# Performance work log

Measured on AMD Instinct MI355X. Metric: run time of the kernel, lower is better.

## Reference

```python
import jax, jax.numpy as jnp
import numpy as np

N_NODES = 50000


def setup_inputs() -> dict:
    key = jax.random.key(0)
    ks = jax.random.split(key, 6)
    d_in, d_out = 256, 256
    n_edges = 1_600_000
    x = jax.random.normal(ks[0], (N_NODES, d_in), dtype=jnp.float32)
    edge_index = jax.random.randint(ks[1], (2, n_edges), 0, N_NODES, dtype=jnp.int64)
    edge_attr = jax.random.normal(ks[2], (n_edges, 16), dtype=jnp.float32)  # unused by forward
    W1 = jax.random.normal(ks[3], (d_in, d_out), dtype=jnp.float32) * (1.0 / np.sqrt(d_in))
    b1 = jnp.zeros((d_out,), dtype=jnp.float32)
    W2 = jax.random.normal(ks[4], (d_out, d_out), dtype=jnp.float32) * (1.0 / np.sqrt(d_out))
    b2 = jnp.zeros((d_out,), dtype=jnp.float32)
    eps = jnp.zeros((1,), dtype=jnp.float32)  # train_eps=True, init 0
    return {"x": x, "edge_index": edge_index, "edge_attr": edge_attr,
            "W1": W1, "b1": b1, "W2": W2, "b2": b2, "eps": eps}


def reference(x, edge_index, edge_attr, W1, b1, W2, b2, eps):
    src, dst = edge_index[0], edge_index[1]
    # sum aggregation: agg[i] = sum_{(j->i) in E} x[j]
    agg = jax.ops.segment_sum(x[src], dst, num_segments=N_NODES)  # [N, d_in]
    h = (1.0 + eps[0]) * x + agg
    # MLP: Linear -> ReLU -> (dropout=0) -> Linear
    h = jax.nn.relu(h @ W1 + b1)
    out = h @ W2 + b2
    return out
```

## Files before the change

kernel.cpp:

```cpp
#include <hip/hip_runtime.h>
#include <stdint.h>

#define NODES 50000
#define D 256
#define MP 50048
#define NBUCK 196
#define CAP 10240
#define EPB 4096
#define HS_LD 264
#define CAST_BLOCKS 12500

typedef short bf16x8 __attribute__((ext_vector_type(8)));
typedef float f32x4 __attribute__((ext_vector_type(4)));

__device__ inline unsigned short f2b(float f) {
    unsigned int u = __float_as_uint(f);
    unsigned int r = (u + 0x7fffu + ((u >> 16) & 1u)) >> 16;
    return (unsigned short)r;
}

__device__ inline bool ei_is64(const int* ei) {
    return (ei[1] | ei[3] | ei[5] | ei[7]) == 0;
}
__device__ inline int ei_get(const int* __restrict__ ei, long long pos, bool is64) {
    return is64 ? ei[2 * pos] : ei[(int)pos];
}

__global__ __launch_bounds__(256) void prep_kernel(const float* __restrict__ x,
                                                   unsigned short* __restrict__ xb,
                                                   int* __restrict__ bcnt,
                                                   const float* __restrict__ W1,
                                                   const float* __restrict__ W2,
                                                   unsigned short* __restrict__ P1,
                                                   unsigned short* __restrict__ P2) {
    int blk = blockIdx.x;
    if (blk < CAST_BLOCKS) {
        if (blk == 0 && threadIdx.x < NBUCK) bcnt[threadIdx.x] = 0;
        int t = blk * 256 + threadIdx.x;
        float4 v = ((const float4*)x)[t];
        unsigned int lo = (unsigned int)f2b(v.x) | ((unsigned int)f2b(v.y) << 16);
        unsigned int hi = (unsigned int)f2b(v.z) | ((unsigned int)f2b(v.w) << 16);
        ((uint2*)xb)[t] = make_uint2(lo, hi);
    } else {
        int t = (blk - CAST_BLOCKS) * 256 + threadIdx.x;
        const float* W = (t < 8192) ? W1 : W2;
        unsigned short* P = (t < 8192) ? P1 : P2;
        int u = t & 8191;
        int lane = u & 63, nt = (u >> 6) & 15, s = u >> 10;
        int q = lane >> 4, n = nt * 16 + (lane & 15);
        int kbase = s * 32 + q * 8;
#pragma unroll
        for (int j = 0; j < 8; j++) P[u * 8 + j] = f2b(W[(kbase + j) * D + n]);
    }
}

__global__ __launch_bounds__(256) void partA_kernel(const int* __restrict__ ei, int E,
                                                    int* __restrict__ bcnt,
                                                    unsigned int* __restrict__ ebufT) {
    __shared__ int cnt[256];
    __shared__ int gbase[256];
    __shared__ int lcur[256];
    bool is64 = ei_is64(ei);
    int tid = threadIdx.x;
    cnt[tid] = 0;
    lcur[tid] = 0;
    __syncthreads();
    long long pairBase = ((long long)blockIdx.x * EPB) >> 1;
    unsigned int w[16];
    int bk[16];
#pragma unroll
    for (int r = 0; r < 8; r++) {
        long long pp = pairBase + (long long)r * 256 + tid;
        long long e0 = pp * 2;
        int s0 = 0, s1 = 0, d0 = 0, d1 = 0;
        bool v1 = (e0 + 1 < E), v0 = (e0 < E);
        if (v1) {
            if (is64) {
                uint4 sv = *(const uint4*)(ei + 4 * pp);
                uint4 dv = *(const uint4*)(ei + (size_t)2 * E + 4 * pp);
                s0 = (int)sv.x; s1 = (int)sv.z; d0 = (int)dv.x; d1 = (int)dv.z;
            } else {
                uint2 sv = *(const uint2*)(ei + 2 * pp);
                uint2 dv = *(const uint2*)(ei + (size_t)E + 2 * pp);
                s0 = (int)sv.x; s1 = (int)sv.y; d0 = (int)dv.x; d1 = (int)dv.y;
            }
        } else if (v0) {
            s0 = ei_get(ei, e0, is64);
            d0 = ei_get(ei, (long long)E + e0, is64);
        }
        bk[2 * r] = v0 ? (d0 >> 8) : -1;
        bk[2 * r + 1] = v1 ? (d1 >> 8) : -1;
        w[2 * r] = ((unsigned int)(d0 & 255) << 16) | (unsigned int)s0;
        w[2 * r + 1] = ((unsigned int)(d1 & 255) << 16) | (unsigned int)s1;
        if (v0) atomicAdd(&cnt[bk[2 * r]], 1);
        if (v1) atomicAdd(&cnt[bk[2 * r + 1]], 1);
    }
    __syncthreads();
    if (tid < NBUCK && cnt[tid] > 0) gbase[tid] = atomicAdd(&bcnt[tid], cnt[tid]);
    __syncthreads();
#pragma unroll
    for (int r = 0; r < 16; r++) {
        if (bk[r] >= 0) {
            int p = atomicAdd(&lcur[bk[r]], 1);
            ebufT[(size_t)bk[r] * CAP + gbase[bk[r]] + p] = w[r];
        }
    }
}

__global__ __launch_bounds__(256) void bscan_kernel(const int* __restrict__ bcnt,
                                                    int* __restrict__ bstart,
                                                    int* __restrict__ offs, int E) {
    __shared__ int buf[256];
    int tid = threadIdx.x;
    int v = (tid < NBUCK) ? bcnt[tid] : 0;
    buf[tid] = v;
    __syncthreads();
    for (int off = 1; off < 256; off <<= 1) {
        int xv = (tid >= off) ? buf[tid - off] : 0;
        __syncthreads();
        buf[tid] += xv;
        __syncthreads();
    }
    if (tid < NBUCK) bstart[tid] = buf[tid] - v;
    if (tid == 0) offs[NODES] = E;
}

__global__ __launch_bounds__(1024) void partB_kernel(const int* __restrict__ bcnt,
                                                     const int* __restrict__ bstart,
                                                     const unsigned int* __restrict__ ebufT,
                                                     int* __restrict__ offs,
                                                     int* __restrict__ ebuf) {
    __shared__ int ncnt[256];
    __shared__ int ncur[256];
    int b = blockIdx.x, tid = threadIdx.x;
    int n = bcnt[b];
    int base = bstart[b];
    if (tid < 256) ncnt[tid] = 0;
    __syncthreads();
    const unsigned int* reg = ebufT + (size_t)b * CAP;
    for (int i = tid; i < n; i += 1024) atomicAdd(&ncnt[reg[i] >> 16], 1);
    __syncthreads();
    int v = 0;
    if (tid < 256) {
        v = ncnt[tid];
        ncur[tid] = v;
    }
    __syncthreads();
    for (int off = 1; off < 256; off <<= 1) {
        int xv = 0;
        if (tid < 256 && tid >= off) xv = ncur[tid - off];
        __syncthreads();
        if (tid < 256) ncur[tid] += xv;
        __syncthreads();
    }
    if (tid < 256) {
        int excl = ncur[tid] - v;
        int node = b * 256 + tid;
        if (node < NODES) offs[node] = base + excl;
        ncur[tid] = excl;
    }
    __syncthreads();
    for (int i = tid; i < n; i += 1024) {
        unsigned int w = reg[i];
        int p = atomicAdd(&ncur[w >> 16], 1);
        ebuf[base + p] = (int)(w & 0xffffu);
    }
}

__device__ inline void upk_add(uint4 w, float* a) {
    a[0] += __uint_as_float(w.x << 16);
    a[1] += __uint_as_float(w.x & 0xffff0000u);
    a[2] += __uint_as_float(w.y << 16);
    a[3] += __uint_as_float(w.y & 0xffff0000u);
    a[4] += __uint_as_float(w.z << 16);
    a[5] += __uint_as_float(w.z & 0xffff0000u);
    a[6] += __uint_as_float(w.w << 16);
    a[7] += __uint_as_float(w.w & 0xffff0000u);
}

__global__ __launch_bounds__(256) void agg_kernel(const unsigned short* __restrict__ xb,
                                                  const int* __restrict__ offs,
                                                  const int* __restrict__ ebuf,
                                                  const float* __restrict__ eps,
                                                  unsigned short* __restrict__ h0) {
    int wv = (blockIdx.x * 256 + threadIdx.x) >> 6;
    int lane = threadIdx.x & 63;
    if (wv >= NODES) return;
    int half = lane >> 5;
    int l32 = lane & 31;
    float aA[8] = {0, 0, 0, 0, 0, 0, 0, 0};
    float aB[8] = {0, 0, 0, 0, 0, 0, 0, 0};
    int beg = offs[wv], end = offs[wv + 1];
    int j = beg;
    for (; j + 8 <= end; j += 8) {
        int i0 = ebuf[j + half];
        int i1 = ebuf[j + 2 + half];
        int i2 = ebuf[j + 4 + half];
        int i3 = ebuf[j + 6 + half];
        uint4 w0 = *(const uint4*)(xb + (size_t)i0 * D + l32 * 8);
        uint4 w1 = *(const uint4*)(xb + (size_t)i1 * D + l32 * 8);
        uint4 w2 = *(const uint4*)(xb + (size_t)i2 * D + l32 * 8);
        uint4 w3 = *(const uint4*)(xb + (size_t)i3 * D + l32 * 8);
        upk_add(w0, aA);
        upk_add(w1, aB);
        upk_add(w2, aA);
        upk_add(w3, aB);
    }
    for (; j + 2 <= end; j += 2) {
        int i0 = ebuf[j + half];
        uint4 w0 = *(const uint4*)(xb + (size_t)i0 * D + l32 * 8);
        upk_add(w0, aA);
    }
    if (j < end && half == 0) {
        int i0 = ebuf[j];
        uint4 w0 = *(const uint4*)(xb + (size_t)i0 * D + l32 * 8);
        upk_add(w0, aA);
    }
    float a[8];
#pragma unroll
    for (int i = 0; i < 8; i++) {
        a[i] = aA[i] + aB[i];
        a[i] += __shfl_xor(a[i], 32);
    }
    if (half == 0) {
        float scale = 1.0f + eps[0];
        uint4 v = *(const uint4*)(xb + (size_t)wv * D + l32 * 8);
        a[0] += scale * __uint_as_float(v.x << 16);
        a[1] += scale * __uint_as_float(v.x & 0xffff0000u);
        a[2] += scale * __uint_as_float(v.y << 16);
        a[3] += scale * __uint_as_float(v.y & 0xffff0000u);
        a[4] += scale * __uint_as_float(v.z << 16);
        a[5] += scale * __uint_as_float(v.z & 0xffff0000u);
        a[6] += scale * __uint_as_float(v.w << 16);
        a[7] += scale * __uint_as_float(v.w & 0xffff0000u);
        uint4 o;
        o.x = (unsigned int)f2b(a[0]) | ((unsigned int)f2b(a[1]) << 16);
        o.y = (unsigned int)f2b(a[2]) | ((unsigned int)f2b(a[3]) << 16);
        o.z = (unsigned int)f2b(a[4]) | ((unsigned int)f2b(a[5]) << 16);
        o.w = (unsigned int)f2b(a[6]) | ((unsigned int)f2b(a[7]) << 16);
        ((uint4*)(h0 + (size_t)wv * D))[l32] = o;
    }
}

__global__ __launch_bounds__(256) void gemm_fused_kernel(const unsigned short* __restrict__ A,
                                                         const unsigned short* __restrict__ P1,
                                                         const float* __restrict__ b1,
                                                         const unsigned short* __restrict__ P2,
                                                         const float* __restrict__ b2,
                                                         float* __restrict__ out, int Mvalid) {
    __shared__ unsigned short hs[64 * HS_LD];
    int wv = threadIdx.x >> 6;
    int lane = threadIdx.x & 63;
    int quad = lane >> 4, l16 = lane & 15;
    int mBase = blockIdx.x * 64;
    const bf16x8* B1v = (const bf16x8*)P1;
    const bf16x8* B2v = (const bf16x8*)P2;

    {
        f32x4 acc[4][4] = {};
#pragma unroll
        for (int ks = 0; ks < 8; ks++) {
            bf16x8 af[4], bf[4];
#pragma unroll
            for (int mi = 0; mi < 4; mi++) {
                int row = mBase + mi * 16 + l16;
                af[mi] = *(const bf16x8*)(A + (size_t)row * D + ks * 32 + quad * 8);
            }
#pragma unroll
            for (int ni = 0; ni < 4; ni++) bf[ni] = B1v[(ks * 16 + wv * 4 + ni) * 64 + lane];
#pragma unroll
            for (int mi = 0; mi < 4; mi++)
#pragma unroll
                for (int ni = 0; ni < 4; ni++)
                    acc[mi][ni] = __builtin_amdgcn_mfma_f32_16x16x32_bf16(af[mi], bf[ni],
                                                                          acc[mi][ni], 0, 0, 0);
        }
#pragma unroll
        for (int mi = 0; mi < 4; mi++)
#pragma unroll
            for (int ni = 0; ni < 4; ni++) {
                int col = wv * 64 + ni * 16 + l16;
                float bs = b1[col];
#pragma unroll
                for (int r = 0; r < 4; r++) {
                    int rl = mi * 16 + quad * 4 + r;
                    hs[rl * HS_LD + col] = f2b(fmaxf(acc[mi][ni][r] + bs, 0.0f));
                }
            }
    }
    __syncthreads();

    f32x4 acc[4][4] = {};
#pragma unroll
    for (int ks = 0; ks < 8; ks++) {
        bf16x8 af[4], bf[4];
#pragma unroll
        for (int mi = 0; mi < 4; mi++)
            af[mi] = *(const bf16x8*)(hs + (mi * 16 + l16) * HS_LD + ks * 32 + quad * 8);
#pragma unroll
        for (int ni = 0; ni < 4; ni++) bf[ni] = B2v[(ks * 16 + wv * 4 + ni) * 64 + lane];
#pragma unroll
        for (int mi = 0; mi < 4; mi++)
#pragma unroll
            for (int ni = 0; ni < 4; ni++)
                acc[mi][ni] =
                    __builtin_amdgcn_mfma_f32_16x16x32_bf16(af[mi], bf[ni], acc[mi][ni], 0, 0, 0);
    }
#pragma unroll
    for (int mi = 0; mi < 4; mi++)
#pragma unroll
        for (int ni = 0; ni < 4; ni++) {
            int col = wv * 64 + ni * 16 + l16;
            float bs = b2[col];
#pragma unroll
            for (int r = 0; r < 4; r++) {
                int row = mBase + mi * 16 + quad * 4 + r;
                if (row < Mvalid) out[(size_t)row * D + col] = acc[mi][ni][r] + bs;
            }
        }
}

extern "C" void kernel_launch(void* const* d_in, const int* in_sizes, int n_in,
                              void* d_out, int out_size, void* d_ws, size_t ws_size,
                              hipStream_t stream) {
    const float* x = (const float*)d_in[0];
    const int* ei = (const int*)d_in[1];
    const float* W1 = (const float*)d_in[3];
    const float* b1 = (const float*)d_in[4];
    const float* W2 = (const float*)d_in[5];
    const float* b2 = (const float*)d_in[6];
    const float* eps = (const float*)d_in[7];
    int E = in_sizes[1] / 2;

    char* p = (char*)d_ws;
    auto alloc = [&](size_t bytes) {
        char* r = p;
        p += (bytes + 255) & ~(size_t)255;
        return r;
    };
    unsigned short* xb = (unsigned short*)alloc((size_t)MP * D * 2);
    unsigned short* h0 = (unsigned short*)alloc((size_t)MP * D * 2);
    unsigned short* P1 = (unsigned short*)alloc(8192 * 8 * 2);
    unsigned short* P2 = (unsigned short*)alloc(8192 * 8 * 2);
    int* bcnt = (int*)alloc((size_t)NBUCK * 4);
    int* bstart = (int*)alloc((size_t)(NBUCK + 1) * 4);
    int* offs = (int*)alloc((size_t)(NODES + 1) * 4);
    int* ebuf = (int*)alloc((size_t)E * 4);
    unsigned int* ebufT = (unsigned int*)alloc((size_t)NBUCK * CAP * 4);

    prep_kernel<<<CAST_BLOCKS + 64, 256, 0, stream>>>(x, xb, bcnt, W1, W2, P1, P2);
    partA_kernel<<<(E + EPB - 1) / EPB, 256, 0, stream>>>(ei, E, bcnt, ebufT);
    bscan_kernel<<<1, 256, 0, stream>>>(bcnt, bstart, offs, E);
    partB_kernel<<<NBUCK, 1024, 0, stream>>>(bcnt, bstart, ebufT, offs, ebuf);
    agg_kernel<<<(NODES + 3) / 4, 256, 0, stream>>>(xb, offs, ebuf, eps, h0);
    gemm_fused_kernel<<<MP / 64, 256, 0, stream>>>(h0, P1, b1, P2, b2, (float*)d_out, NODES);
}
```

Baseline: 364.4 us.

## Split aggregation into two column-half passes and fold bucket scan into partB

```diff
diff --git a/kernel.cpp b/kernel.cpp
--- a/kernel.cpp
+++ b/kernel.cpp
@@ -32,10 +32,12 @@
                                                    const float* __restrict__ W1,
                                                    const float* __restrict__ W2,
                                                    unsigned short* __restrict__ P1,
-                                                   unsigned short* __restrict__ P2) {
+                                                   unsigned short* __restrict__ P2,
+                                                   int* __restrict__ offs, int E) {
     int blk = blockIdx.x;
     if (blk < CAST_BLOCKS) {
         if (blk == 0 && threadIdx.x < NBUCK) bcnt[threadIdx.x] = 0;
+        if (blk == 0 && threadIdx.x == 0) offs[NODES] = E;
         int t = blk * 256 + threadIdx.x;
         float4 v = ((const float4*)x)[t];
         unsigned int lo = (unsigned int)f2b(v.x) | ((unsigned int)f2b(v.y) << 16);
@@ -107,36 +109,28 @@
     }
 }
 
-__global__ __launch_bounds__(256) void bscan_kernel(const int* __restrict__ bcnt,
-                                                    int* __restrict__ bstart,
-                                                    int* __restrict__ offs, int E) {
-    __shared__ int buf[256];
-    int tid = threadIdx.x;
-    int v = (tid < NBUCK) ? bcnt[tid] : 0;
-    buf[tid] = v;
-    __syncthreads();
-    for (int off = 1; off < 256; off <<= 1) {
-        int xv = (tid >= off) ? buf[tid - off] : 0;
-        __syncthreads();
-        buf[tid] += xv;
-        __syncthreads();
-    }
-    if (tid < NBUCK) bstart[tid] = buf[tid] - v;
-    if (tid == 0) offs[NODES] = E;
-}
-
 __global__ __launch_bounds__(1024) void partB_kernel(const int* __restrict__ bcnt,
-                                                     const int* __restrict__ bstart,
                                                      const unsigned int* __restrict__ ebufT,
                                                      int* __restrict__ offs,
                                                      int* __restrict__ ebuf) {
+    __shared__ int sb[256];
     __shared__ int ncnt[256];
     __shared__ int ncur[256];
     int b = blockIdx.x, tid = threadIdx.x;
+    if (tid < 256) {
+        sb[tid] = (tid < NBUCK) ? bcnt[tid] : 0;
+        ncnt[tid] = 0;
+    }
+    __syncthreads();
+    for (int off = 1; off < 256; off <<= 1) {
+        int xv = 0;
+        if (tid < 256 && tid >= off) xv = sb[tid - off];
+        __syncthreads();
+        if (tid < 256) sb[tid] += xv;
+        __syncthreads();
+    }
     int n = bcnt[b];
-    int base = bstart[b];
-    if (tid < 256) ncnt[tid] = 0;
-    __syncthreads();
+    int base = sb[b] - n;
     const unsigned int* reg = ebufT + (size_t)b * CAP;
     for (int i = tid; i < n; i += 1024) atomicAdd(&ncnt[reg[i] >> 16], 1);
     __syncthreads();
@@ -182,49 +176,44 @@
                                                   const int* __restrict__ offs,
                                                   const int* __restrict__ ebuf,
                                                   const float* __restrict__ eps,
-                                                  unsigned short* __restrict__ h0) {
+                                                  unsigned short* __restrict__ h0, int colOff) {
     int wv = (blockIdx.x * 256 + threadIdx.x) >> 6;
     int lane = threadIdx.x & 63;
     if (wv >= NODES) return;
-    int half = lane >> 5;
-    int l32 = lane & 31;
+    int g = lane >> 4, l16 = lane & 15;
+    const unsigned short* colBase = xb + colOff + l16 * 8;
     float aA[8] = {0, 0, 0, 0, 0, 0, 0, 0};
     float aB[8] = {0, 0, 0, 0, 0, 0, 0, 0};
     int beg = offs[wv], end = offs[wv + 1];
     int j = beg;
     for (; j + 8 <= end; j += 8) {
-        int i0 = ebuf[j + half];
-        int i1 = ebuf[j + 2 + half];
-        int i2 = ebuf[j + 4 + half];
-        int i3 = ebuf[j + 6 + half];
-        uint4 w0 = *(const uint4*)(xb + (size_t)i0 * D + l32 * 8);
-        uint4 w1 = *(const uint4*)(xb + (size_t)i1 * D + l32 * 8);
-        uint4 w2 = *(const uint4*)(xb + (size_t)i2 * D + l32 * 8);
-        uint4 w3 = *(const uint4*)(xb + (size_t)i3 * D + l32 * 8);
+        int i0 = ebuf[j + g];
+        int i1 = ebuf[j + 4 + g];
+        uint4 w0 = *(const uint4*)(colBase + (size_t)i0 * D);
+        uint4 w1 = *(const uint4*)(colBase + (size_t)i1 * D);
         upk_add(w0, aA);
         upk_add(w1, aB);
-        upk_add(w2, aA);
-        upk_add(w3, aB);
-    }
-    for (; j + 2 <= end; j += 2) {
-        int i0 = ebuf[j + half];
-        uint4 w0 = *(const uint4*)(xb + (size_t)i0 * D + l32 * 8);
+    }
+    for (; j + 4 <= end; j += 4) {
+        int i0 = ebuf[j + g];
+        uint4 w0 = *(const uint4*)(colBase + (size_t)i0 * D);
         upk_add(w0, aA);
     }
-    if (j < end && half == 0) {
-        int i0 = ebuf[j];
-        uint4 w0 = *(const uint4*)(xb + (size_t)i0 * D + l32 * 8);
+    if (j + g < end) {
+        int i0 = ebuf[j + g];
+        uint4 w0 = *(const uint4*)(colBase + (size_t)i0 * D);
         upk_add(w0, aA);
     }
     float a[8];
 #pragma unroll
     for (int i = 0; i < 8; i++) {
         a[i] = aA[i] + aB[i];
+        a[i] += __shfl_xor(a[i], 16);
         a[i] += __shfl_xor(a[i], 32);
     }
-    if (half == 0) {
+    if (g == 0) {
         float scale = 1.0f + eps[0];
-        uint4 v = *(const uint4*)(xb + (size_t)wv * D + l32 * 8);
+        uint4 v = *(const uint4*)(xb + (size_t)wv * D + colOff + l16 * 8);
         a[0] += scale * __uint_as_float(v.x << 16);
         a[1] += scale * __uint_as_float(v.x & 0xffff0000u);
         a[2] += scale * __uint_as_float(v.y << 16);
@@ -238,7 +227,7 @@
         o.y = (unsigned int)f2b(a[2]) | ((unsigned int)f2b(a[3]) << 16);
         o.z = (unsigned int)f2b(a[4]) | ((unsigned int)f2b(a[5]) << 16);
         o.w = (unsigned int)f2b(a[6]) | ((unsigned int)f2b(a[7]) << 16);
-        ((uint4*)(h0 + (size_t)wv * D))[l32] = o;
+        ((uint4*)(h0 + (size_t)wv * D + colOff))[l16] = o;
     }
 }
 
@@ -343,15 +332,14 @@
     unsigned short* P1 = (unsigned short*)alloc(8192 * 8 * 2);
     unsigned short* P2 = (unsigned short*)alloc(8192 * 8 * 2);
     int* bcnt = (int*)alloc((size_t)NBUCK * 4);
-    int* bstart = (int*)alloc((size_t)(NBUCK + 1) * 4);
     int* offs = (int*)alloc((size_t)(NODES + 1) * 4);
     int* ebuf = (int*)alloc((size_t)E * 4);
     unsigned int* ebufT = (unsigned int*)alloc((size_t)NBUCK * CAP * 4);
 
-    prep_kernel<<<CAST_BLOCKS + 64, 256, 0, stream>>>(x, xb, bcnt, W1, W2, P1, P2);
+    prep_kernel<<<CAST_BLOCKS + 64, 256, 0, stream>>>(x, xb, bcnt, W1, W2, P1, P2, offs, E);
     partA_kernel<<<(E + EPB - 1) / EPB, 256, 0, stream>>>(ei, E, bcnt, ebufT);
-    bscan_kernel<<<1, 256, 0, stream>>>(bcnt, bstart, offs, E);
-    partB_kernel<<<NBUCK, 1024, 0, stream>>>(bcnt, bstart, ebufT, offs, ebuf);
-    agg_kernel<<<(NODES + 3) / 4, 256, 0, stream>>>(xb, offs, ebuf, eps, h0);
+    partB_kernel<<<NBUCK, 1024, 0, stream>>>(bcnt, ebufT, offs, ebuf);
+    agg_kernel<<<(NODES + 3) / 4, 256, 0, stream>>>(xb, offs, ebuf, eps, h0, 0);
+    agg_kernel<<<(NODES + 3) / 4, 256, 0, stream>>>(xb, offs, ebuf, eps, h0, 128);
     gemm_fused_kernel<<<MP / 64, 256, 0, stream>>>(h0, P1, b1, P2, b2, (float*)d_out, NODES);
 }
```

Result: no change. 357.9 us (-1.8%).
